# Performance work log

Measured on AMD Instinct MI355X. Metric: run time of the kernel, lower is better.

## Reference

```python
import jax, jax.numpy as jnp
import numpy as np
import math

B, S, V = 16, 128, 32000
D_MODEL, D_STATE, L, T = 1024, 512, 2, 4
TAU, THR = 2.0, 1.0
DECAY = math.exp(-1.0 / TAU)  # membrane decay exp(-1/tau)
EPS = 1e-5
ALPHA = 2.0  # ATan surrogate alpha


@jax.custom_vjp
def atan_spike(x):
    # spikingjelly surrogate.ATan: heaviside forward, atan-derivative backward
    return (x >= 0.0).astype(x.dtype)

def _atan_fwd(x):
    return atan_spike(x), x

def _atan_bwd(x, g):
    return (g * (ALPHA / 2.0) / (1.0 + (jnp.pi / 2.0 * ALPHA * x) ** 2),)

atan_spike.defvjp(_atan_fwd, _atan_bwd)


def lif(mem, x):
    # AdaptiveLIFNeuron in eval mode: threshold fixed at base_threshold=1.0
    mem_t = mem * DECAY + x
    spike = atan_spike(mem_t - THR)
    return mem_t * (1.0 - spike), spike  # soft-ish reset: mem*(1-spike)


def layernorm(x, g, b):
    m = jnp.mean(x, -1, keepdims=True)
    v = jnp.mean((x - m) ** 2, -1, keepdims=True)
    return (x - m) * jax.lax.rsqrt(v + EPS) * g + b


def setup_inputs() -> dict:
    key = jax.random.key(0)
    ks = jax.random.split(key, 8)

    def w(k, shape, fan_in):
        return (jax.random.normal(k, shape, jnp.float32) / np.sqrt(fan_in).astype(np.float32))

    return {
        "input_ids": jax.random.randint(ks[0], (B, S), 0, V),
        "emb_table": jax.random.normal(ks[1], (V, D_MODEL), jnp.float32) * 0.02,
        "W_enc": w(ks[2], (D_MODEL, D_MODEL), D_MODEL),
        "b_enc": jnp.zeros((D_MODEL,), jnp.float32),
        "ln_s_g": jnp.ones((L, D_STATE), jnp.float32),
        "ln_s_b": jnp.zeros((L, D_STATE), jnp.float32),
        "Wg": w(ks[3], (L, D_STATE, D_MODEL), D_STATE),
        "bg": jnp.zeros((L, D_MODEL), jnp.float32),
        "ln_e_g": jnp.ones((L, D_MODEL), jnp.float32),
        "ln_e_b": jnp.zeros((L, D_MODEL), jnp.float32),
        "Wi": w(ks[4], (L, D_MODEL, D_STATE), D_MODEL),
        "bi": jnp.zeros((L, D_STATE), jnp.float32),
        "W_out": w(ks[5], (D_STATE, V), D_STATE),
        "b_out": jnp.zeros((V,), jnp.float32),
    }


def reference(input_ids, emb_table, W_enc, b_enc, ln_s_g, ln_s_b, Wg, bg,
              ln_e_g, ln_e_b, Wi, bi, W_out, b_out):
    token_emb = emb_table[input_ids]           # [B,S,D_MODEL]
    emb_seq = jnp.swapaxes(token_emb, 0, 1)    # [S,B,D_MODEL]

    init = (
        jnp.zeros((L, B, D_STATE), jnp.float32),  # top-down states per layer
        jnp.zeros((B, D_MODEL), jnp.float32),      # input-encoder LIF mem
        jnp.zeros((L, B, D_MODEL), jnp.float32),   # generative LIF mems
        jnp.zeros((L, B, D_STATE), jnp.float32),   # inference LIF mems
    )

    def token_step(carry, emb_t):
        states, enc_mem, gen_mems, inf_mems = carry
        # input encoder: Linear + LIF; bottom_up_input is the spike output
        enc_mem, bottom = lif(enc_mem, emb_t @ W_enc + b_enc)
        for _t in range(T):
            for j in range(L):
                s = states[j]
                # generative pathway: prediction from top-down state
                pre = layernorm(s, ln_s_g[j], ln_s_b[j]) @ Wg[j] + bg[j]
                gm, pred = lif(gen_mems[j], pre)
                gen_mems = gen_mems.at[j].set(gm)
                error = bottom - pred
                # inference pathway: state update from prediction error
                inf_in = layernorm(error, ln_e_g[j], ln_e_b[j]) @ Wi[j] + bi[j]
                im, upd = lif(inf_mems[j], inf_in)
                inf_mems = inf_mems.at[j].set(im)
                states = states.at[j].set(s + upd)
                bottom = error  # error propagates upward / across timesteps
        return (states, enc_mem, gen_mems, inf_mems), states[L - 1]

    _, hs = jax.lax.scan(token_step, init, emb_seq)  # [S,B,D_STATE]
    hs = jnp.swapaxes(hs, 0, 1)                      # [B,S,D_STATE]
    return hs @ W_out + b_out                        # logits [B,S,V]
```

## Files before the change

kernel.cpp:

```cpp
#include <hip/hip_runtime.h>
#include <math.h>

#define NWG 256
#define TPB 256

typedef float v4f __attribute__((ext_vector_type(4)));

constexpr int Bn = 16, Sn = 128, Vn = 32000, DMn = 1024, DSn = 512;
constexpr float DECAYc = 0.6065306597126334f;
constexpr float THRc = 1.0f, EPSc = 1e-5f;

constexpr size_t OF_FLAGS  = 0;
constexpr size_t OF_STATES = (size_t)256*4096;
constexpr size_t OF_E0     = OF_STATES + (size_t)2*16*512*4;
constexpr size_t OF_E1     = OF_E0 + (size_t)16*1024*4;
constexpr size_t OF_ENCX   = OF_E1 + (size_t)16*1024*4;
constexpr size_t OF_HS     = OF_ENCX + (size_t)128*16*1024*4;
constexpr size_t OF_WGT    = OF_HS + (size_t)128*16*512*4;
constexpr size_t OF_WIT    = OF_WGT + (size_t)2*1024*512*4;
constexpr size_t INIT_BYTES = OF_E0;

struct SP {
  const int* ids; const float* emb;
  const float* W_enc; const float* b_enc;
  const float* ln_s_g; const float* ln_s_b;
  const float* Wg; const float* bg;
  const float* ln_e_g; const float* ln_e_b;
  const float* Wi; const float* bi;
};

__device__ __forceinline__ void st_cg(float* p, float v) {
  __hip_atomic_store(p, v, __ATOMIC_RELAXED, __HIP_MEMORY_SCOPE_AGENT);
}
__device__ __forceinline__ int ld_flag(const int* p) {
  return __hip_atomic_load(p, __ATOMIC_RELAXED, __HIP_MEMORY_SCOPE_AGENT);
}
__device__ __forceinline__ void st_flag(int* p, int v) {
  __hip_atomic_store(p, v, __ATOMIC_RELAXED, __HIP_MEMORY_SCOPE_AGENT);
}

__device__ __forceinline__ int swc(int c) { return c ^ ((c >> 3) & 7); }

template<int SZ>
__device__ __forceinline__ void bstep(float* v, bool up, int M) {
  #pragma unroll
  for (int q = 0; q < SZ/2; q++) {
    float lo = v[q], hi = v[q + SZ/2];
    float send = up ? lo : hi;
    float recv = __shfl_xor(send, M);
    v[q] = (up ? hi : lo) + recv;
  }
}

__device__ __forceinline__ void publish(int* myflag, int tid, int epoch) {
  asm volatile("s_waitcnt vmcnt(0)" ::: "memory");
  __syncthreads();
  if (tid == 0) st_flag(myflag, epoch);
}
__device__ __forceinline__ void waithalf(const int* othf, int tid, int target) {
  if (tid < 32) {
    while (ld_flag(othf + tid*1024) < target) { }
  }
  asm volatile("" ::: "memory");
  __syncthreads();
}

template<bool FIRST>
__device__ __forceinline__ void gen_step(
    const float (&wreg)[8][8], const float (&lg)[8], const float (&lb)[8],
    float biasv, const float* __restrict__ src,
    float& mreg, float& btReg, float eEv,
    float* __restrict__ errw, int o, int bg, int grp, float* X, int tid)
{
  const int w = tid >> 6, l = tid & 63;
  v4f xr0, xr1;
  const float* sp = src + (size_t)(grp*4 + w)*DSn + l*8;
  asm volatile("global_load_dwordx4 %0, %1, off sc0 sc1" : "=v"(xr0) : "v"(sp));
  asm volatile("global_load_dwordx4 %0, %1, off sc0 sc1" : "=v"(xr1) : "v"(sp + 4));
  asm volatile("s_waitcnt vmcnt(0)" ::: "memory");
  __builtin_amdgcn_sched_barrier(0);
  float s1 = 0.f;
  #pragma unroll
  for (int e = 0; e < 4; e++) { s1 += xr0[e]; s1 += xr1[e]; }
  #pragma unroll
  for (int off = 32; off; off >>= 1) s1 += __shfl_xor(s1, off);
  const float mean = s1 * (1.0f / 512.0f);
  float s2 = 0.f;
  #pragma unroll
  for (int e = 0; e < 4; e++) {
    float d0 = xr0[e] - mean; s2 += d0*d0;
    float d1 = xr1[e] - mean; s2 += d1*d1;
  }
  #pragma unroll
  for (int off = 32; off; off >>= 1) s2 += __shfl_xor(s2, off);
  const float rstd = 1.0f / sqrtf(s2 * (1.0f / 512.0f) + EPSc);
  v4f ov0, ov1;
  #pragma unroll
  for (int e = 0; e < 4; e++) {
    ov0[e] = (xr0[e] - mean)*rstd*lg[e]   + lb[e];
    ov1[e] = (xr1[e] - mean)*rstd*lg[4+e] + lb[4+e];
  }
  *(v4f*)(X + w*DSn + (swc(l*2 + 0) << 2)) = ov0;
  *(v4f*)(X + w*DSn + (swc(l*2 + 1) << 2)) = ov1;
  __syncthreads();
  const int xo0 = swc(l*2 + 0) << 2, xo1 = swc(l*2 + 1) << 2;
  float v[32];
  #pragma unroll
  for (int n = 0; n < 32; n++) v[n] = 0.f;
  #pragma unroll
  for (int b = 0; b < 4; b++) {
    v4f x0 = *(const v4f*)(X + b*DSn + xo0);
    v4f x1 = *(const v4f*)(X + b*DSn + xo1);
    #pragma unroll
    for (int i = 0; i < 8; i++) {
      float a = v[i*4 + b];
      #pragma unroll
      for (int e = 0; e < 4; e++) a = fmaf(x0[e], wreg[e][i], a);
      #pragma unroll
      for (int e = 0; e < 4; e++) a = fmaf(x1[e], wreg[4+e][i], a);
      v[i*4 + b] = a;
    }
  }
  bstep<32>(v, (l & 32) != 0, 32);
  bstep<16>(v, (l & 16) != 0, 16);
  bstep<8> (v, (l &  8) != 0,  8);
  bstep<4> (v, (l &  4) != 0,  4);
  bstep<2> (v, (l &  2) != 0,  2);
  v[0] += __shfl_xor(v[0], 1);
  const float val = v[0] + biasv;
  const float mt = mreg * DECAYc + val;
  const float spk = (mt >= THRc) ? 1.f : 0.f;
  mreg = mt * (1.f - spk);
  const float ne = (FIRST ? eEv : btReg) - spk;
  btReg = ne;
  if ((l & 1) == 0) st_cg(errw + (size_t)bg*DMn + o, ne);
}

__device__ __forceinline__ void inf_step(
    const float (&wreg)[16][4], const float (&lg)[16], const float (&lb)[16],
    float biasv, const float* __restrict__ src,
    float& mreg, float& streg,
    float* __restrict__ stw, float* __restrict__ hsw,
    int o, int bg, int grp, float* X, int tid)
{
  const int w = tid >> 6, l = tid & 63;
  v4f xr[4];
  const float* sp = src + (size_t)(grp*4 + w)*DMn + l*16;
  #pragma unroll
  for (int q = 0; q < 4; q++)
    asm volatile("global_load_dwordx4 %0, %1, off sc0 sc1" : "=v"(xr[q]) : "v"(sp + 4*q));
  asm volatile("s_waitcnt vmcnt(0)" ::: "memory");
  __builtin_amdgcn_sched_barrier(0);
  float s1 = 0.f;
  #pragma unroll
  for (int q = 0; q < 4; q++)
    #pragma unroll
    for (int e = 0; e < 4; e++) s1 += xr[q][e];
  #pragma unroll
  for (int off = 32; off; off >>= 1) s1 += __shfl_xor(s1, off);
  const float mean = s1 * (1.0f / 1024.0f);
  float s2 = 0.f;
  #pragma unroll
  for (int q = 0; q < 4; q++)
    #pragma unroll
    for (int e = 0; e < 4; e++) { float d = xr[q][e] - mean; s2 += d*d; }
  #pragma unroll
  for (int off = 32; off; off >>= 1) s2 += __shfl_xor(s2, off);
  const float rstd = 1.0f / sqrtf(s2 * (1.0f / 1024.0f) + EPSc);
  #pragma unroll
  for (int q = 0; q < 4; q++) {
    v4f ov;
    #pragma unroll
    for (int e = 0; e < 4; e++)
      ov[e] = (xr[q][e] - mean)*rstd*lg[q*4+e] + lb[q*4+e];
    *(v4f*)(X + w*DMn + (swc(l*4 + q) << 2)) = ov;
  }
  __syncthreads();
  int xo[4];
  #pragma unroll
  for (int q = 0; q < 4; q++) xo[q] = swc(l*4 + q) << 2;
  float v[16];
  #pragma unroll
  for (int n = 0; n < 16; n++) v[n] = 0.f;
  #pragma unroll
  for (int b = 0; b < 4; b++) {
    v4f xv[4];
    #pragma unroll
    for (int q = 0; q < 4; q++) xv[q] = *(const v4f*)(X + b*DMn + xo[q]);
    #pragma unroll
    for (int i = 0; i < 4; i++) {
      float a = v[i*4 + b];
      #pragma unroll
      for (int q = 0; q < 4; q++)
        #pragma unroll
        for (int e = 0; e < 4; e++) a = fmaf(xv[q][e], wreg[q*4+e][i], a);
      v[i*4 + b] = a;
    }
  }
  bstep<16>(v, (l & 32) != 0, 32);
  bstep<8> (v, (l & 16) != 0, 16);
  bstep<4> (v, (l &  8) != 0,  8);
  bstep<2> (v, (l &  4) != 0,  4);
  v[0] += __shfl_xor(v[0], 2);
  v[0] += __shfl_xor(v[0], 1);
  const float val = v[0] + biasv;
  const float mt = mreg * DECAYc + val;
  const float spk = (mt >= THRc) ? 1.f : 0.f;
  mreg = mt * (1.f - spk);
  const float ns = streg + spk;
  streg = ns;
  if ((l & 3) == 0) {
    st_cg(stw + (size_t)bg*DSn + o, ns);
    if (hsw) hsw[(size_t)bg*DSn + o] = ns;
  }
}

__global__ void __launch_bounds__(TPB, 1) snn_scan(SP p, char* __restrict__ ws)
{
  extern __shared__ float X[];
  const int wgg = blockIdx.x, tid = threadIdx.x;
  const int grp = wgg >> 6, wgl = wgg & 63;
  const int w = tid >> 6, l = tid & 63;
  int* flags  = (int*)(ws + OF_FLAGS);
  int* myflag = flags + (size_t)wgg*1024;
  float* states = (float*)(ws + OF_STATES);
  float* e0     = (float*)(ws + OF_E0);
  float* e1     = (float*)(ws + OF_E1);
  const float* encX = (const float*)(ws + OF_ENCX);
  float* hs     = (float*)(ws + OF_HS);
  const float* WgT = (const float*)(ws + OF_WGT);
  const float* WiT = (const float*)(ws + OF_WIT);
  float* st0 = states;
  float* st1 = states + (size_t)Bn*DSn;

  if (wgl < 32) {
    const int* othf = flags + (size_t)(grp*64 + 32)*1024;
    const int o0 = wgl * 32;
    const int o_i = (l >> 3) & 7, b_loc = (l >> 1) & 3;
    const int o = o0 + w*8 + o_i, bg = grp*4 + b_loc;
    float wA[8][8], wB[8][8];
    #pragma unroll
    for (int i = 0; i < 8; i++) {
      const v4f* pa = (const v4f*)(WgT + (size_t)(o0 + w*8 + i)*DSn + l*8);
      const v4f* pb = (const v4f*)(WgT + (size_t)DMn*DSn + (size_t)(o0 + w*8 + i)*DSn + l*8);
      v4f a0 = pa[0], a1 = pa[1], b0 = pb[0], b1 = pb[1];
      #pragma unroll
      for (int e = 0; e < 4; e++) {
        wA[e][i] = a0[e]; wA[4+e][i] = a1[e];
        wB[e][i] = b0[e]; wB[4+e][i] = b1[e];
      }
    }
    float lgA[8], lbA[8], lgB[8], lbB[8];
    {
      const v4f* g0 = (const v4f*)(p.ln_s_g + l*8);
      const v4f* c0 = (const v4f*)(p.ln_s_b + l*8);
      const v4f* g1 = (const v4f*)(p.ln_s_g + DSn + l*8);
      const v4f* c1 = (const v4f*)(p.ln_s_b + DSn + l*8);
      v4f ga = g0[0], gb = g0[1], ba = c0[0], bb = c0[1];
      v4f gc = g1[0], gd = g1[1], bc = c1[0], bd = c1[1];
      #pragma unroll
      for (int e = 0; e < 4; e++) {
        lgA[e] = ga[e]; lgA[4+e] = gb[e]; lbA[e] = ba[e]; lbA[4+e] = bb[e];
        lgB[e] = gc[e]; lgB[4+e] = gd[e]; lbB[e] = bc[e]; lbB[4+e] = bd[e];
      }
    }
    const float biasA = p.bg[o], biasB = p.bg[DMn + o];
    float encMem = 0.f, btReg = 0.f, genMemA = 0.f, genMemB = 0.f;

    for (int s = 0; s < Sn; s++) {
      const int s8 = s*8;
      const float ex = encX[(size_t)s*Bn*DMn + (size_t)bg*DMn + o];
      const float emt = encMem*DECAYc + ex;
      const float esp = (emt >= THRc) ? 1.f : 0.f;
      encMem = emt * (1.f - esp);
      waithalf(othf, tid, s8 - 1);
      gen_step<true >(wA, lgA, lbA, biasA, st0, genMemA, btReg, esp, e0, o, bg, grp, X, tid);
      publish(myflag, tid, s8 + 1);
      waithalf(othf, tid, s8 + 0);
      gen_step<false>(wB, lgB, lbB, biasB, st1, genMemB, btReg, 0.f, e1, o, bg, grp, X, tid);
      publish(myflag, tid, s8 + 2);
      waithalf(othf, tid, s8 + 1);
      gen_step<false>(wA, lgA, lbA, biasA, st0, genMemA, btReg, 0.f, e0, o, bg, grp, X, tid);
      publish(myflag, tid, s8 + 3);
      waithalf(othf, tid, s8 + 2);
      gen_step<false>(wB, lgB, lbB, biasB, st1, genMemB, btReg, 0.f, e1, o, bg, grp, X, tid);
      publish(myflag, tid, s8 + 4);
      waithalf(othf, tid, s8 + 3);
      gen_step<false>(wA, lgA, lbA, biasA, st0, genMemA, btReg, 0.f, e0, o, bg, grp, X, tid);
      publish(myflag, tid, s8 + 5);
      waithalf(othf, tid, s8 + 4);
      gen_step<false>(wB, lgB, lbB, biasB, st1, genMemB, btReg, 0.f, e1, o, bg, grp, X, tid);
      publish(myflag, tid, s8 + 6);
      waithalf(othf, tid, s8 + 5);
      gen_step<false>(wA, lgA, lbA, biasA, st0, genMemA, btReg, 0.f, e0, o, bg, grp, X, tid);
      publish(myflag, tid, s8 + 7);
      waithalf(othf, tid, s8 + 6);
      gen_step<false>(wB, lgB, lbB, biasB, st1, genMemB, btReg, 0.f, e1, o, bg, grp, X, tid);
      publish(myflag, tid, s8 + 8);
    }
  } else {
    const int* othf = flags + (size_t)(grp*64)*1024;
    const int o0 = (wgl - 32) * 16;
    const int o_i = (l >> 4) & 3, b_loc = (l >> 2) & 3;
    const int o = o0 + w*4 + o_i, bg = grp*4 + b_loc;
    float wA[16][4], wB[16][4];
    #pragma unroll
    for (int i = 0; i < 4; i++) {
      const v4f* pa = (const v4f*)(WiT + (size_t)(o0 + w*4 + i)*DMn + l*16);
      const v4f* pb = (const v4f*)(WiT + (size_t)DSn*DMn + (size_t)(o0 + w*4 + i)*DMn + l*16);
      #pragma unroll
      for (int q = 0; q < 4; q++) {
        v4f a = pa[q], b = pb[q];
        #pragma unroll
        for (int e = 0; e < 4; e++) { wA[q*4+e][i] = a[e]; wB[q*4+e][i] = b[e]; }
      }
    }
    float lgA[16], lbA[16], lgB[16], lbB[16];
    {
      const v4f* g0 = (const v4f*)(p.ln_e_g + l*16);
      const v4f* c0 = (const v4f*)(p.ln_e_b + l*16);
      const v4f* g1 = (const v4f*)(p.ln_e_g + DMn + l*16);
      const v4f* c1 = (const v4f*)(p.ln_e_b + DMn + l*16);
      #pragma unroll
      for (int q = 0; q < 4; q++) {
        v4f ga = g0[q], ba = c0[q], gb = g1[q], bb = c1[q];
        #pragma unroll
        for (int e = 0; e < 4; e++) {
          lgA[q*4+e] = ga[e]; lbA[q*4+e] = ba[e];
          lgB[q*4+e] = gb[e]; lbB[q*4+e] = bb[e];
        }
      }
    }
    const float biasA = p.bi[o], biasB = p.bi[DSn + o];
    float infMemA = 0.f, infMemB = 0.f, stRegA = 0.f, stRegB = 0.f;

    for (int s = 0; s < Sn; s++) {
      const int s8 = s*8;
      waithalf(othf, tid, s8 + 1);
      inf_step(wA, lgA, lbA, biasA, e0, infMemA, stRegA, st0, nullptr, o, bg, grp, X, tid);
      publish(myflag, tid, s8 + 1);
      waithalf(othf, tid, s8 + 2);
      inf_step(wB, lgB, lbB, biasB, e1, infMemB, stRegB, st1, nullptr, o, bg, grp, X, tid);
      publish(myflag, tid, s8 + 2);
      waithalf(othf, tid, s8 + 3);
      inf_step(wA, lgA, lbA, biasA, e0, infMemA, stRegA, st0, nullptr, o, bg, grp, X, tid);
      publish(myflag, tid, s8 + 3);
      waithalf(othf, tid, s8 + 4);
      inf_step(wB, lgB, lbB, biasB, e1, infMemB, stRegB, st1, nullptr, o, bg, grp, X, tid);
      publish(myflag, tid, s8 + 4);
      waithalf(othf, tid, s8 + 5);
      inf_step(wA, lgA, lbA, biasA, e0, infMemA, stRegA, st0, nullptr, o, bg, grp, X, tid);
      publish(myflag, tid, s8 + 5);
      waithalf(othf, tid, s8 + 6);
      inf_step(wB, lgB, lbB, biasB, e1, infMemB, stRegB, st1, nullptr, o, bg, grp, X, tid);
      publish(myflag, tid, s8 + 6);
      waithalf(othf, tid, s8 + 7);
      inf_step(wA, lgA, lbA, biasA, e0, infMemA, stRegA, st0, nullptr, o, bg, grp, X, tid);
      publish(myflag, tid, s8 + 7);
      waithalf(othf, tid, s8 + 8);
      inf_step(wB, lgB, lbB, biasB, e1, infMemB, stRegB, st1,
               hs + (size_t)s*Bn*DSn, o, bg, grp, X, tid);
      publish(myflag, tid, s8 + 8);
    }
  }
}

__global__ void __launch_bounds__(256) transpose_k(
    const float* __restrict__ in, float* __restrict__ out, int K, int O)
{
  __shared__ float t[32][33];
  const int ob = blockIdx.x * 32, kb = blockIdx.y * 32;
  const int x = threadIdx.x, y = threadIdx.y;
  #pragma unroll
  for (int i = 0; i < 32; i += 8) t[y + i][x] = in[(size_t)(kb + y + i)*O + ob + x];
  __syncthreads();
  #pragma unroll
  for (int i = 0; i < 32; i += 8) out[(size_t)(ob + y + i)*K + kb + x] = t[x][y + i];
}

__global__ void __launch_bounds__(256) enc_gemm(
    const int* __restrict__ ids, const float* __restrict__ emb,
    const float* __restrict__ We, const float* __restrict__ be,
    float* __restrict__ encX)
{
  __shared__ float As[32][128];
  __shared__ float Bs[32][128];
  __shared__ int rowid[128];
  const int tid = threadIdx.x;
  const int ntile = blockIdx.x * 128;
  const int mtile = blockIdx.y * 128;
  if (tid < 128) {
    int m = mtile + tid;
    rowid[tid] = ids[(m & 15)*Sn + (m >> 4)];
  }
  __syncthreads();
  const int tx = tid & 15, ty = tid >> 4;
  float acc[8][8];
  #pragma unroll
  for (int i = 0; i < 8; i++)
    #pragma unroll
    for (int q = 0; q < 8; q++) acc[i][q] = 0.f;

  for (int kb = 0; kb < 32; kb++) {
    #pragma unroll
    for (int r = 0; r < 4; r++) {
      int idx = tid + r*256;
      int m = idx >> 3, kq = idx & 7;
      float4 a = *(const float4*)(emb + (size_t)rowid[m]*DMn + kb*32 + kq*4);
      As[kq*4+0][m] = a.x; As[kq*4+1][m] = a.y;
      As[kq*4+2][m] = a.z; As[kq*4+3][m] = a.w;
    }
    #pragma unroll
    for (int r = 0; r < 4; r++) {
      int idx = tid + r*256;
      int k = idx >> 5, nq = idx & 31;
      *(float4*)(&Bs[k][nq*4]) =
          *(const float4*)(We + (size_t)(kb*32 + k)*DMn + ntile + nq*4);
    }
    __syncthreads();
    #pragma unroll
    for (int k = 0; k < 32; k++) {
      float4 a0 = *(float4*)(&As[k][ty*8]);
      float4 a1 = *(float4*)(&As[k][ty*8+4]);
      float4 b0 = *(float4*)(&Bs[k][tx*8]);
      float4 b1 = *(float4*)(&Bs[k][tx*8+4]);
      float av[8] = {a0.x,a0.y,a0.z,a0.w,a1.x,a1.y,a1.z,a1.w};
      float bv[8] = {b0.x,b0.y,b0.z,b0.w,b1.x,b1.y,b1.z,b1.w};
      #pragma unroll
      for (int i = 0; i < 8; i++)
        #pragma unroll
        for (int q = 0; q < 8; q++) acc[i][q] += av[i]*bv[q];
    }
    __syncthreads();
  }
  const float* bop = be + ntile + tx*8;
  float4 bv0 = *(const float4*)bop;
  float4 bv1 = *(const float4*)(bop + 4);
  #pragma unroll
  for (int i = 0; i < 8; i++) {
    int m = mtile + ty*8 + i;
    float* op = encX + (size_t)m*DMn + ntile + tx*8;
    float4 v0 = make_float4(acc[i][0]+bv0.x, acc[i][1]+bv0.y,
                            acc[i][2]+bv0.z, acc[i][3]+bv0.w);
    float4 v1 = make_float4(acc[i][4]+bv1.x, acc[i][5]+bv1.y,
                            acc[i][6]+bv1.z, acc[i][7]+bv1.w);
    *(float4*)op = v0;
    *(float4*)(op + 4) = v1;
  }
}

__global__ void __launch_bounds__(256) out_gemm(
    const float* __restrict__ hs, const float* __restrict__ Wo,
    const float* __restrict__ bo, float* __restrict__ out)
{
  __shared__ float As[32][128];
  __shared__ float Bs[32][128];
  const int tid = threadIdx.x;
  const int ntile = blockIdx.x * 128;
  const int mtile = blockIdx.y * 128;
  const int tx = tid & 15, ty = tid >> 4;
  float acc[8][8];
  #pragma unroll
  for (int i = 0; i < 8; i++)
    #pragma unroll
    for (int q = 0; q < 8; q++) acc[i][q] = 0.f;

  for (int kb = 0; kb < 16; kb++) {
    #pragma unroll
    for (int r = 0; r < 4; r++) {
      int idx = tid + r*256;
      int m = idx >> 3, kq = idx & 7;
      float4 a = *(const float4*)(hs + (size_t)(mtile + m)*512 + kb*32 + kq*4);
      As[kq*4+0][m] = a.x; As[kq*4+1][m] = a.y;
      As[kq*4+2][m] = a.z; As[kq*4+3][m] = a.w;
    }
    #pragma unroll
    for (int r = 0; r < 4; r++) {
      int idx = tid + r*256;
      int k = idx >> 5, nq = idx & 31;
      *(float4*)(&Bs[k][nq*4]) =
          *(const float4*)(Wo + (size_t)(kb*32 + k)*Vn + ntile + nq*4);
    }
    __syncthreads();
    #pragma unroll
    for (int k = 0; k < 32; k++) {
      float4 a0 = *(float4*)(&As[k][ty*8]);
      float4 a1 = *(float4*)(&As[k][ty*8+4]);
      float4 b0 = *(float4*)(&Bs[k][tx*8]);
      float4 b1 = *(float4*)(&Bs[k][tx*8+4]);
      float av[8] = {a0.x,a0.y,a0.z,a0.w,a1.x,a1.y,a1.z,a1.w};
      float bv[8] = {b0.x,b0.y,b0.z,b0.w,b1.x,b1.y,b1.z,b1.w};
      #pragma unroll
      for (int i = 0; i < 8; i++)
        #pragma unroll
        for (int q = 0; q < 8; q++) acc[i][q] += av[i]*bv[q];
    }
    __syncthreads();
  }
  const float* bop = bo + ntile + tx*8;
  float4 bv0 = *(const float4*)bop;
  float4 bv1 = *(const float4*)(bop + 4);
  #pragma unroll
  for (int i = 0; i < 8; i++) {
    int m = mtile + ty*8 + i;
    float* op = out + ((size_t)(m & 15)*Sn + (m >> 4))*Vn + ntile + tx*8;
    float4 v0 = make_float4(acc[i][0]+bv0.x, acc[i][1]+bv0.y,
                            acc[i][2]+bv0.z, acc[i][3]+bv0.w);
    float4 v1 = make_float4(acc[i][4]+bv1.x, acc[i][5]+bv1.y,
                            acc[i][6]+bv1.z, acc[i][7]+bv1.w);
    *(float4*)op = v0;
    *(float4*)(op + 4) = v1;
  }
}

extern "C" void kernel_launch(void* const* d_in, const int* in_sizes, int n_in,
                              void* d_out, int out_size, void* d_ws, size_t ws_size,
                              hipStream_t stream) {
  (void)in_sizes; (void)n_in; (void)out_size; (void)ws_size;
  SP p;
  p.ids    = (const int*)  d_in[0];
  p.emb    = (const float*)d_in[1];
  p.W_enc  = (const float*)d_in[2];
  p.b_enc  = (const float*)d_in[3];
  p.ln_s_g = (const float*)d_in[4];
  p.ln_s_b = (const float*)d_in[5];
  p.Wg     = (const float*)d_in[6];
  p.bg     = (const float*)d_in[7];
  p.ln_e_g = (const float*)d_in[8];
  p.ln_e_b = (const float*)d_in[9];
  p.Wi     = (const float*)d_in[10];
  p.bi     = (const float*)d_in[11];
  const float* Wo = (const float*)d_in[12];
  const float* bo = (const float*)d_in[13];

  char* ws = (char*)d_ws;
  float* WgT  = (float*)(ws + OF_WGT);
  float* WiT  = (float*)(ws + OF_WIT);
  float* encX = (float*)(ws + OF_ENCX);
  float* hs   = (float*)(ws + OF_HS);

  hipMemsetAsync(ws, 0, INIT_BYTES, stream);

  hipLaunchKernelGGL(transpose_k, dim3(32, 16), dim3(32, 8), 0, stream,
                     p.Wg, WgT, 512, 1024);
  hipLaunchKernelGGL(transpose_k, dim3(32, 16), dim3(32, 8), 0, stream,
                     p.Wg + (size_t)512*1024, WgT + (size_t)1024*512, 512, 1024);
  hipLaunchKernelGGL(transpose_k, dim3(16, 32), dim3(32, 8), 0, stream,
                     p.Wi, WiT, 1024, 512);
  hipLaunchKernelGGL(transpose_k, dim3(16, 32), dim3(32, 8), 0, stream,
                     p.Wi + (size_t)1024*512, WiT + (size_t)512*1024, 1024, 512);

  hipLaunchKernelGGL(enc_gemm, dim3(DMn/128, 2048/128), dim3(256), 0, stream,
                     p.ids, p.emb, p.W_enc, p.b_enc, encX);

  hipLaunchKernelGGL(snn_scan, dim3(NWG), dim3(TPB), 86016, stream, p, ws);

  hipLaunchKernelGGL(out_gemm, dim3(Vn/128, 2048/128), dim3(256), 0, stream,
                     hs, Wo, bo, (float*)d_out);
}
```

Measured before the change: 4.528 ms.

## Switch persistent scan to per-wave flag sync, drop LDS staging and register-resident weights

Synchronisation moves from workgroup level to wave level. Each wave publishes its own flag and polls 128 peer-wave flags with a wave-wide __all, so __syncthreads is gone. Each wave now loads all four batch rows and computes the layernorm for them redundantly, so the normalised activations no longer go through LDS. Weights and LN parameters are reloaded from global memory (likely cache-resident) every step instead of being pinned in registers. This frees VGPRs and removes block barriers, but adds redundant loads, extra layernorm work and heavier flag polling traffic.

```diff
diff --git a/kernel.cpp b/kernel.cpp
--- a/kernel.cpp
+++ b/kernel.cpp
@@ -39,8 +39,6 @@
   __hip_atomic_store(p, v, __ATOMIC_RELAXED, __HIP_MEMORY_SCOPE_AGENT);
 }
 
-__device__ __forceinline__ int swc(int c) { return c ^ ((c >> 3) & 7); }
-
 template<int SZ>
 __device__ __forceinline__ void bstep(float* v, bool up, int M) {
   #pragma unroll
@@ -52,75 +50,93 @@
   }
 }
 
-__device__ __forceinline__ void publish(int* myflag, int tid, int epoch) {
+__device__ __forceinline__ void waitwaves(const int* fl, int l, int target) {
+  const int* p0 = fl + (size_t)l * 256;
+  const int* p1 = fl + (size_t)(l + 64) * 256;
+  for (;;) {
+    int a = ld_flag(p0);
+    int b = ld_flag(p1);
+    if (__all((a >= target) && (b >= target))) break;
+  }
+  asm volatile("" ::: "memory");
+}
+__device__ __forceinline__ void pubwave(int* myflag, int l, int epoch) {
   asm volatile("s_waitcnt vmcnt(0)" ::: "memory");
-  __syncthreads();
-  if (tid == 0) st_flag(myflag, epoch);
-}
-__device__ __forceinline__ void waithalf(const int* othf, int tid, int target) {
-  if (tid < 32) {
-    while (ld_flag(othf + tid*1024) < target) { }
-  }
-  asm volatile("" ::: "memory");
-  __syncthreads();
+  if (l == 0) st_flag(myflag, epoch);
 }
 
 template<bool FIRST>
 __device__ __forceinline__ void gen_step(
-    const float (&wreg)[8][8], const float (&lg)[8], const float (&lb)[8],
-    float biasv, const float* __restrict__ src,
+    const float* __restrict__ Wbase,
+    const float (&lg)[8], const float (&lb)[8], float biasv,
+    const float* __restrict__ src,
+    const int* __restrict__ othf, int target,
+    int* __restrict__ myflag, int epoch,
     float& mreg, float& btReg, float eEv,
-    float* __restrict__ errw, int o, int bg, int grp, float* X, int tid)
+    float* __restrict__ errw,
+    int o0w, int o, int bg, int grp, int l)
 {
-  const int w = tid >> 6, l = tid & 63;
-  v4f xr0, xr1;
-  const float* sp = src + (size_t)(grp*4 + w)*DSn + l*8;
-  asm volatile("global_load_dwordx4 %0, %1, off sc0 sc1" : "=v"(xr0) : "v"(sp));
-  asm volatile("global_load_dwordx4 %0, %1, off sc0 sc1" : "=v"(xr1) : "v"(sp + 4));
+  v4f wv[8][2];
+  #pragma unroll
+  for (int i = 0; i < 8; i++) {
+    const v4f* wp = (const v4f*)(Wbase + (size_t)(o0w + i)*DSn + l*8);
+    wv[i][0] = wp[0]; wv[i][1] = wp[1];
+  }
+  waitwaves(othf, l, target);
+  v4f x[4][2];
+  #pragma unroll
+  for (int r = 0; r < 4; r++) {
+    const float* sp = src + (size_t)(grp*4 + r)*DSn + l*8;
+    asm volatile("global_load_dwordx4 %0, %1, off sc0 sc1" : "=v"(x[r][0]) : "v"(sp));
+    asm volatile("global_load_dwordx4 %0, %1, off sc0 sc1" : "=v"(x[r][1]) : "v"(sp + 4));
+  }
   asm volatile("s_waitcnt vmcnt(0)" ::: "memory");
   __builtin_amdgcn_sched_barrier(0);
-  float s1 = 0.f;
-  #pragma unroll
-  for (int e = 0; e < 4; e++) { s1 += xr0[e]; s1 += xr1[e]; }
-  #pragma unroll
-  for (int off = 32; off; off >>= 1) s1 += __shfl_xor(s1, off);
-  const float mean = s1 * (1.0f / 512.0f);
-  float s2 = 0.f;
-  #pragma unroll
-  for (int e = 0; e < 4; e++) {
-    float d0 = xr0[e] - mean; s2 += d0*d0;
-    float d1 = xr1[e] - mean; s2 += d1*d1;
-  }
-  #pragma unroll
-  for (int off = 32; off; off >>= 1) s2 += __shfl_xor(s2, off);
-  const float rstd = 1.0f / sqrtf(s2 * (1.0f / 512.0f) + EPSc);
-  v4f ov0, ov1;
-  #pragma unroll
-  for (int e = 0; e < 4; e++) {
-    ov0[e] = (xr0[e] - mean)*rstd*lg[e]   + lb[e];
-    ov1[e] = (xr1[e] - mean)*rstd*lg[4+e] + lb[4+e];
-  }
-  *(v4f*)(X + w*DSn + (swc(l*2 + 0) << 2)) = ov0;
-  *(v4f*)(X + w*DSn + (swc(l*2 + 1) << 2)) = ov1;
-  __syncthreads();
-  const int xo0 = swc(l*2 + 0) << 2, xo1 = swc(l*2 + 1) << 2;
+  float s1[4] = {0.f,0.f,0.f,0.f}, s2[4], mean[4], rstd[4];
+  #pragma unroll
+  for (int r = 0; r < 4; r++)
+    #pragma unroll
+    for (int e = 0; e < 4; e++) { s1[r] += x[r][0][e]; s1[r] += x[r][1][e]; }
+  #pragma unroll
+  for (int off = 32; off; off >>= 1)
+    #pragma unroll
+    for (int r = 0; r < 4; r++) s1[r] += __shfl_xor(s1[r], off);
+  #pragma unroll
+  for (int r = 0; r < 4; r++) { mean[r] = s1[r] * (1.0f/512.0f); s2[r] = 0.f; }
+  #pragma unroll
+  for (int r = 0; r < 4; r++)
+    #pragma unroll
+    for (int e = 0; e < 4; e++) {
+      float d0 = x[r][0][e] - mean[r]; s2[r] += d0*d0;
+      float d1 = x[r][1][e] - mean[r]; s2[r] += d1*d1;
+    }
+  #pragma unroll
+  for (int off = 32; off; off >>= 1)
+    #pragma unroll
+    for (int r = 0; r < 4; r++) s2[r] += __shfl_xor(s2[r], off);
+  #pragma unroll
+  for (int r = 0; r < 4; r++) rstd[r] = 1.0f / sqrtf(s2[r]*(1.0f/512.0f) + EPSc);
+  #pragma unroll
+  for (int r = 0; r < 4; r++)
+    #pragma unroll
+    for (int e = 0; e < 4; e++) {
+      x[r][0][e] = (x[r][0][e] - mean[r])*rstd[r]*lg[e]   + lb[e];
+      x[r][1][e] = (x[r][1][e] - mean[r])*rstd[r]*lg[4+e] + lb[4+e];
+    }
   float v[32];
   #pragma unroll
   for (int n = 0; n < 32; n++) v[n] = 0.f;
   #pragma unroll
-  for (int b = 0; b < 4; b++) {
-    v4f x0 = *(const v4f*)(X + b*DSn + xo0);
-    v4f x1 = *(const v4f*)(X + b*DSn + xo1);
+  for (int b = 0; b < 4; b++)
     #pragma unroll
     for (int i = 0; i < 8; i++) {
       float a = v[i*4 + b];
       #pragma unroll
-      for (int e = 0; e < 4; e++) a = fmaf(x0[e], wreg[e][i], a);
-      #pragma unroll
-      for (int e = 0; e < 4; e++) a = fmaf(x1[e], wreg[4+e][i], a);
+      for (int e = 0; e < 4; e++) a = fmaf(x[b][0][e], wv[i][0][e], a);
+      #pragma unroll
+      for (int e = 0; e < 4; e++) a = fmaf(x[b][1][e], wv[i][1][e], a);
       v[i*4 + b] = a;
     }
-  }
   bstep<32>(v, (l & 32) != 0, 32);
   bstep<16>(v, (l & 16) != 0, 16);
   bstep<8> (v, (l &  8) != 0,  8);
@@ -134,69 +150,90 @@
   const float ne = (FIRST ? eEv : btReg) - spk;
   btReg = ne;
   if ((l & 1) == 0) st_cg(errw + (size_t)bg*DMn + o, ne);
+  pubwave(myflag, l, epoch);
 }
 
 __device__ __forceinline__ void inf_step(
-    const float (&wreg)[16][4], const float (&lg)[16], const float (&lb)[16],
-    float biasv, const float* __restrict__ src,
+    const float* __restrict__ Wbase,
+    const float* __restrict__ lngp, const float* __restrict__ lnbp, float biasv,
+    const float* __restrict__ src,
+    const int* __restrict__ othf, int target,
+    int* __restrict__ myflag, int epoch,
     float& mreg, float& streg,
     float* __restrict__ stw, float* __restrict__ hsw,
-    int o, int bg, int grp, float* X, int tid)
+    int o0w, int o, int bg, int grp, int l)
 {
-  const int w = tid >> 6, l = tid & 63;
-  v4f xr[4];
-  const float* sp = src + (size_t)(grp*4 + w)*DMn + l*16;
-  #pragma unroll
-  for (int q = 0; q < 4; q++)
-    asm volatile("global_load_dwordx4 %0, %1, off sc0 sc1" : "=v"(xr[q]) : "v"(sp + 4*q));
+  v4f wv[4][4];
+  #pragma unroll
+  for (int i = 0; i < 4; i++) {
+    const v4f* wp = (const v4f*)(Wbase + (size_t)(o0w + i)*DMn + l*16);
+    #pragma unroll
+    for (int q = 0; q < 4; q++) wv[i][q] = wp[q];
+  }
+  v4f lgv[4], lbv[4];
+  {
+    const v4f* g = (const v4f*)(lngp + l*16);
+    const v4f* c = (const v4f*)(lnbp + l*16);
+    #pragma unroll
+    for (int q = 0; q < 4; q++) { lgv[q] = g[q]; lbv[q] = c[q]; }
+  }
+  waitwaves(othf, l, target);
+  v4f x[4][4];
+  #pragma unroll
+  for (int r = 0; r < 4; r++) {
+    const float* sp = src + (size_t)(grp*4 + r)*DMn + l*16;
+    #pragma unroll
+    for (int q = 0; q < 4; q++)
+      asm volatile("global_load_dwordx4 %0, %1, off sc0 sc1" : "=v"(x[r][q]) : "v"(sp + 4*q));
+  }
   asm volatile("s_waitcnt vmcnt(0)" ::: "memory");
   __builtin_amdgcn_sched_barrier(0);
-  float s1 = 0.f;
-  #pragma unroll
-  for (int q = 0; q < 4; q++)
-    #pragma unroll
-    for (int e = 0; e < 4; e++) s1 += xr[q][e];
-  #pragma unroll
-  for (int off = 32; off; off >>= 1) s1 += __shfl_xor(s1, off);
-  const float mean = s1 * (1.0f / 1024.0f);
-  float s2 = 0.f;
-  #pragma unroll
-  for (int q = 0; q < 4; q++)
-    #pragma unroll
-    for (int e = 0; e < 4; e++) { float d = xr[q][e] - mean; s2 += d*d; }
-  #pragma unroll
-  for (int off = 32; off; off >>= 1) s2 += __shfl_xor(s2, off);
-  const float rstd = 1.0f / sqrtf(s2 * (1.0f / 1024.0f) + EPSc);
-  #pragma unroll
-  for (int q = 0; q < 4; q++) {
-    v4f ov;
-    #pragma unroll
-    for (int e = 0; e < 4; e++)
-      ov[e] = (xr[q][e] - mean)*rstd*lg[q*4+e] + lb[q*4+e];
-    *(v4f*)(X + w*DMn + (swc(l*4 + q) << 2)) = ov;
-  }
-  __syncthreads();
-  int xo[4];
-  #pragma unroll
-  for (int q = 0; q < 4; q++) xo[q] = swc(l*4 + q) << 2;
+  float s1[4] = {0.f,0.f,0.f,0.f}, s2[4], mean[4], rstd[4];
+  #pragma unroll
+  for (int r = 0; r < 4; r++)
+    #pragma unroll
+    for (int q = 0; q < 4; q++)
+      #pragma unroll
+      for (int e = 0; e < 4; e++) s1[r] += x[r][q][e];
+  #pragma unroll
+  for (int off = 32; off; off >>= 1)
+    #pragma unroll
+    for (int r = 0; r < 4; r++) s1[r] += __shfl_xor(s1[r], off);
+  #pragma unroll
+  for (int r = 0; r < 4; r++) { mean[r] = s1[r] * (1.0f/1024.0f); s2[r] = 0.f; }
+  #pragma unroll
+  for (int r = 0; r < 4; r++)
+    #pragma unroll
+    for (int q = 0; q < 4; q++)
+      #pragma unroll
+      for (int e = 0; e < 4; e++) { float d = x[r][q][e] - mean[r]; s2[r] += d*d; }
+  #pragma unroll
+  for (int off = 32; off; off >>= 1)
+    #pragma unroll
+    for (int r = 0; r < 4; r++) s2[r] += __shfl_xor(s2[r], off);
+  #pragma unroll
+  for (int r = 0; r < 4; r++) rstd[r] = 1.0f / sqrtf(s2[r]*(1.0f/1024.0f) + EPSc);
+  #pragma unroll
+  for (int r = 0; r < 4; r++)
+    #pragma unroll
+    for (int q = 0; q < 4; q++)
+      #pragma unroll
+      for (int e = 0; e < 4; e++)
+        x[r][q][e] = (x[r][q][e] - mean[r])*rstd[r]*lgv[q][e] + lbv[q][e];
   float v[16];
   #pragma unroll
   for (int n = 0; n < 16; n++) v[n] = 0.f;
   #pragma unroll
-  for (int b = 0; b < 4; b++) {
-    v4f xv[4];
-    #pragma unroll
-    for (int q = 0; q < 4; q++) xv[q] = *(const v4f*)(X + b*DMn + xo[q]);
+  for (int b = 0; b < 4; b++)
     #pragma unroll
     for (int i = 0; i < 4; i++) {
       float a = v[i*4 + b];
       #pragma unroll
       for (int q = 0; q < 4; q++)
         #pragma unroll
-        for (int e = 0; e < 4; e++) a = fmaf(xv[q][e], wreg[q*4+e][i], a);
+        for (int e = 0; e < 4; e++) a = fmaf(x[b][q][e], wv[i][q][e], a);
       v[i*4 + b] = a;
     }
-  }
   bstep<16>(v, (l & 32) != 0, 32);
   bstep<8> (v, (l & 16) != 0, 16);
   bstep<4> (v, (l &  8) != 0,  8);
@@ -213,16 +250,18 @@
     st_cg(stw + (size_t)bg*DSn + o, ns);
     if (hsw) hsw[(size_t)bg*DSn + o] = ns;
   }
+  pubwave(myflag, l, epoch);
 }
 
 __global__ void __launch_bounds__(TPB, 1) snn_scan(SP p, char* __restrict__ ws)
 {
-  extern __shared__ float X[];
+  extern __shared__ float Xpad[];
+  (void)Xpad;
   const int wgg = blockIdx.x, tid = threadIdx.x;
   const int grp = wgg >> 6, wgl = wgg & 63;
   const int w = tid >> 6, l = tid & 63;
   int* flags  = (int*)(ws + OF_FLAGS);
-  int* myflag = flags + (size_t)wgg*1024;
+  int* myflag = flags + (size_t)(((grp*64 + wgl) << 2) + w) * 256;
   float* states = (float*)(ws + OF_STATES);
   float* e0     = (float*)(ws + OF_E0);
   float* e1     = (float*)(ws + OF_E1);
@@ -234,22 +273,12 @@
   float* st1 = states + (size_t)Bn*DSn;
 
   if (wgl < 32) {
-    const int* othf = flags + (size_t)(grp*64 + 32)*1024;
-    const int o0 = wgl * 32;
+    const int* othf = flags + (size_t)(grp*256 + 128) * 256;
+    const int o0 = wgl * 32, o0w = o0 + w*8;
     const int o_i = (l >> 3) & 7, b_loc = (l >> 1) & 3;
-    const int o = o0 + w*8 + o_i, bg = grp*4 + b_loc;
-    float wA[8][8], wB[8][8];
-    #pragma unroll
-    for (int i = 0; i < 8; i++) {
-      const v4f* pa = (const v4f*)(WgT + (size_t)(o0 + w*8 + i)*DSn + l*8);
-      const v4f* pb = (const v4f*)(WgT + (size_t)DMn*DSn + (size_t)(o0 + w*8 + i)*DSn + l*8);
-      v4f a0 = pa[0], a1 = pa[1], b0 = pb[0], b1 = pb[1];
-      #pragma unroll
-      for (int e = 0; e < 4; e++) {
-        wA[e][i] = a0[e]; wA[4+e][i] = a1[e];
-        wB[e][i] = b0[e]; wB[4+e][i] = b1[e];
-      }
-    }
+    const int o = o0w + o_i, bg = grp*4 + b_loc;
+    const float* WA = WgT;
+    const float* WB = WgT + (size_t)DMn*DSn;
     float lgA[8], lbA[8], lgB[8], lbB[8];
     {
       const v4f* g0 = (const v4f*)(p.ln_s_g + l*8);
@@ -273,94 +302,51 @@
       const float emt = encMem*DECAYc + ex;
       const float esp = (emt >= THRc) ? 1.f : 0.f;
       encMem = emt * (1.f - esp);
-      waithalf(othf, tid, s8 - 1);
-      gen_step<true >(wA, lgA, lbA, biasA, st0, genMemA, btReg, esp, e0, o, bg, grp, X, tid);
-      publish(myflag, tid, s8 + 1);
-      waithalf(othf, tid, s8 + 0);
-      gen_step<false>(wB, lgB, lbB, biasB, st1, genMemB, btReg, 0.f, e1, o, bg, grp, X, tid);
-      publish(myflag, tid, s8 + 2);
-      waithalf(othf, tid, s8 + 1);
-      gen_step<false>(wA, lgA, lbA, biasA, st0, genMemA, btReg, 0.f, e0, o, bg, grp, X, tid);
-      publish(myflag, tid, s8 + 3);
-      waithalf(othf, tid, s8 + 2);
-      gen_step<false>(wB, lgB, lbB, biasB, st1, genMemB, btReg, 0.f, e1, o, bg, grp, X, tid);
-      publish(myflag, tid, s8 + 4);
-      waithalf(othf, tid, s8 + 3);
-      gen_step<false>(wA, lgA, lbA, biasA, st0, genMemA, btReg, 0.f, e0, o, bg, grp, X, tid);
-      publish(myflag, tid, s8 + 5);
-      waithalf(othf, tid, s8 + 4);
-      gen_step<false>(wB, lgB, lbB, biasB, st1, genMemB, btReg, 0.f, e1, o, bg, grp, X, tid);
-      publish(myflag, tid, s8 + 6);
-      waithalf(othf, tid, s8 + 5);
-      gen_step<false>(wA, lgA, lbA, biasA, st0, genMemA, btReg, 0.f, e0, o, bg, grp, X, tid);
-      publish(myflag, tid, s8 + 7);
-      waithalf(othf, tid, s8 + 6);
-      gen_step<false>(wB, lgB, lbB, biasB, st1, genMemB, btReg, 0.f, e1, o, bg, grp, X, tid);
-      publish(myflag, tid, s8 + 8);
+      gen_step<true >(WA, lgA, lbA, biasA, st0, othf, s8-1, myflag, s8+1,
+                      genMemA, btReg, esp, e0, o0w, o, bg, grp, l);
+      gen_step<false>(WB, lgB, lbB, biasB, st1, othf, s8+0, myflag, s8+2,
+                      genMemB, btReg, 0.f, e1, o0w, o, bg, grp, l);
+      gen_step<false>(WA, lgA, lbA, biasA, st0, othf, s8+1, myflag, s8+3,
+                      genMemA, btReg, 0.f, e0, o0w, o, bg, grp, l);
+      gen_step<false>(WB, lgB, lbB, biasB, st1, othf, s8+2, myflag, s8+4,
+                      genMemB, btReg, 0.f, e1, o0w, o, bg, grp, l);
+      gen_step<false>(WA, lgA, lbA, biasA, st0, othf, s8+3, myflag, s8+5,
+                      genMemA, btReg, 0.f, e0, o0w, o, bg, grp, l);
+      gen_step<false>(WB, lgB, lbB, biasB, st1, othf, s8+4, myflag, s8+6,
+                      genMemB, btReg, 0.f, e1, o0w, o, bg, grp, l);
+      gen_step<false>(WA, lgA, lbA, biasA, st0, othf, s8+5, myflag, s8+7,
+                      genMemA, btReg, 0.f, e0, o0w, o, bg, grp, l);
+      gen_step<false>(WB, lgB, lbB, biasB, st1, othf, s8+6, myflag, s8+8,
+                      genMemB, btReg, 0.f, e1, o0w, o, bg, grp, l);
     }
   } else {
-    const int* othf = flags + (size_t)(grp*64)*1024;
-    const int o0 = (wgl - 32) * 16;
+    const int* othf = flags + (size_t)(grp*256) * 256;
+    const int o0 = (wgl - 32) * 16, o0w = o0 + w*4;
     const int o_i = (l >> 4) & 3, b_loc = (l >> 2) & 3;
-    const int o = o0 + w*4 + o_i, bg = grp*4 + b_loc;
-    float wA[16][4], wB[16][4];
-    #pragma unroll
-    for (int i = 0; i < 4; i++) {
-      const v4f* pa = (const v4f*)(WiT + (size_t)(o0 + w*4 + i)*DMn + l*16);
-      const v4f* pb = (const v4f*)(WiT + (size_t)DSn*DMn + (size_t)(o0 + w*4 + i)*DMn + l*16);
-      #pragma unroll
-      for (int q = 0; q < 4; q++) {
-        v4f a = pa[q], b = pb[q];
-        #pragma unroll
-        for (int e = 0; e < 4; e++) { wA[q*4+e][i] = a[e]; wB[q*4+e][i] = b[e]; }
-      }
-    }
-    float lgA[16], lbA[16], lgB[16], lbB[16];
-    {
-      const v4f* g0 = (const v4f*)(p.ln_e_g + l*16);
-      const v4f* c0 = (const v4f*)(p.ln_e_b + l*16);
-      const v4f* g1 = (const v4f*)(p.ln_e_g + DMn + l*16);
-      const v4f* c1 = (const v4f*)(p.ln_e_b + DMn + l*16);
-      #pragma unroll
-      for (int q = 0; q < 4; q++) {
-        v4f ga = g0[q], ba = c0[q], gb = g1[q], bb = c1[q];
-        #pragma unroll
-        for (int e = 0; e < 4; e++) {
-          lgA[q*4+e] = ga[e]; lbA[q*4+e] = ba[e];
-          lgB[q*4+e] = gb[e]; lbB[q*4+e] = bb[e];
-        }
-      }
-    }
+    const int o = o0w + o_i, bg = grp*4 + b_loc;
+    const float* WA = WiT;
+    const float* WB = WiT + (size_t)DSn*DMn;
     const float biasA = p.bi[o], biasB = p.bi[DSn + o];
     float infMemA = 0.f, infMemB = 0.f, stRegA = 0.f, stRegB = 0.f;
 
     for (int s = 0; s < Sn; s++) {
       const int s8 = s*8;
-      waithalf(othf, tid, s8 + 1);
-      inf_step(wA, lgA, lbA, biasA, e0, infMemA, stRegA, st0, nullptr, o, bg, grp, X, tid);
-      publish(myflag, tid, s8 + 1);
-      waithalf(othf, tid, s8 + 2);
-      inf_step(wB, lgB, lbB, biasB, e1, infMemB, stRegB, st1, nullptr, o, bg, grp, X, tid);
-      publish(myflag, tid, s8 + 2);
-      waithalf(othf, tid, s8 + 3);
-      inf_step(wA, lgA, lbA, biasA, e0, infMemA, stRegA, st0, nullptr, o, bg, grp, X, tid);
-      publish(myflag, tid, s8 + 3);
-      waithalf(othf, tid, s8 + 4);
-      inf_step(wB, lgB, lbB, biasB, e1, infMemB, stRegB, st1, nullptr, o, bg, grp, X, tid);
-      publish(myflag, tid, s8 + 4);
-      waithalf(othf, tid, s8 + 5);
-      inf_step(wA, lgA, lbA, biasA, e0, infMemA, stRegA, st0, nullptr, o, bg, grp, X, tid);
-      publish(myflag, tid, s8 + 5);
-      waithalf(othf, tid, s8 + 6);
-      inf_step(wB, lgB, lbB, biasB, e1, infMemB, stRegB, st1, nullptr, o, bg, grp, X, tid);
-      publish(myflag, tid, s8 + 6);
-      waithalf(othf, tid, s8 + 7);
-      inf_step(wA, lgA, lbA, biasA, e0, infMemA, stRegA, st0, nullptr, o, bg, grp, X, tid);
-      publish(myflag, tid, s8 + 7);
-      waithalf(othf, tid, s8 + 8);
-      inf_step(wB, lgB, lbB, biasB, e1, infMemB, stRegB, st1,
-               hs + (size_t)s*Bn*DSn, o, bg, grp, X, tid);
-      publish(myflag, tid, s8 + 8);
+      inf_step(WA, p.ln_e_g,       p.ln_e_b,       biasA, e0, othf, s8+1, myflag, s8+1,
+               infMemA, stRegA, st0, nullptr, o0w, o, bg, grp, l);
+      inf_step(WB, p.ln_e_g + DMn, p.ln_e_b + DMn, biasB, e1, othf, s8+2, myflag, s8+2,
+               infMemB, stRegB, st1, nullptr, o0w, o, bg, grp, l);
+      inf_step(WA, p.ln_e_g,       p.ln_e_b,       biasA, e0, othf, s8+3, myflag, s8+3,
+               infMemA, stRegA, st0, nullptr, o0w, o, bg, grp, l);
+      inf_step(WB, p.ln_e_g + DMn, p.ln_e_b + DMn, biasB, e1, othf, s8+4, myflag, s8+4,
+               infMemB, stRegB, st1, nullptr, o0w, o, bg, grp, l);
+      inf_step(WA, p.ln_e_g,       p.ln_e_b,       biasA, e0, othf, s8+5, myflag, s8+5,
+               infMemA, stRegA, st0, nullptr, o0w, o, bg, grp, l);
+      inf_step(WB, p.ln_e_g + DMn, p.ln_e_b + DMn, biasB, e1, othf, s8+6, myflag, s8+6,
+               infMemB, stRegB, st1, nullptr, o0w, o, bg, grp, l);
+      inf_step(WA, p.ln_e_g,       p.ln_e_b,       biasA, e0, othf, s8+7, myflag, s8+7,
+               infMemA, stRegA, st0, nullptr, o0w, o, bg, grp, l);
+      inf_step(WB, p.ln_e_g + DMn, p.ln_e_b + DMn, biasB, e1, othf, s8+8, myflag, s8+8,
+               infMemB, stRegB, st1, hs + (size_t)s*Bn*DSn, o0w, o, bg, grp, l);
     }
   }
 }
```

After: 8.673 ms. 91.6% more time.
